# Performance work log

Measured on AMD Instinct MI355X. Metric: run time of the kernel, lower is better.

## Reference

```python
import jax, jax.numpy as jnp
import numpy as np

EPS = 1e-5

def fps(xyz, npoint):
    # iterative farthest point sampling, deterministic start at index 0
    B, N, _ = xyz.shape
    def step(carry, _):
        distance, farthest = carry
        centroid = jnp.take_along_axis(xyz, farthest[:, None, None], axis=1)  # [B,1,3]
        dist = jnp.sum((xyz - centroid) ** 2, -1)                              # [B,N]
        distance = jnp.minimum(distance, dist)
        new_far = jnp.argmax(distance, -1)
        return (distance, new_far), farthest
    init = (jnp.full((B, N), 1e10, xyz.dtype), jnp.zeros((B,), jnp.int32))
    _, idx = jax.lax.scan(step, init, None, length=npoint)
    return idx.T  # [B, npoint]

def gather_points(points, idx):
    # points [B,N,C], idx [B,S] or [B,S,K] -> gathered along N
    B = points.shape[0]
    if idx.ndim == 2:
        return jnp.take_along_axis(points, idx[..., None], axis=1)
    S, K = idx.shape[1], idx.shape[2]
    flat = jnp.take_along_axis(points, idx.reshape(B, S * K)[..., None], axis=1)
    return flat.reshape(B, S, K, points.shape[-1])

def conv_bn_relu(x, W, b, gamma, beta):
    # x [B,C,K,S]; 1x1 conv = channel matmul; BN over (B,K,S) with batch stats
    y = jnp.einsum('bcks,oc->boks', x, W) + b[None, :, None, None]
    mean = jnp.mean(y, axis=(0, 2, 3), keepdims=True)
    var = jnp.mean((y - mean) ** 2, axis=(0, 2, 3), keepdims=True)
    y = (y - mean) * jax.lax.rsqrt(var + EPS)
    y = y * gamma[None, :, None, None] + beta[None, :, None, None]
    return jax.nn.relu(y)

NPOINT = 1024
NSAMPLE = 16

def setup_inputs() -> dict:
    key = jax.random.key(0)
    ks = jax.random.split(key, 6)
    B, N, D = 16, 4096, 128
    C_in, C1, C2 = D + 3, 256, 256
    xyz = jax.random.normal(ks[0], (B, N, 3), dtype=jnp.float32)
    points = jax.random.normal(ks[1], (B, N, D), dtype=jnp.float32)
    W1 = jax.random.normal(ks[2], (C1, C_in), dtype=jnp.float32) / np.sqrt(C_in)
    b1 = jnp.zeros((C1,), jnp.float32)
    g1 = jnp.ones((C1,), jnp.float32)
    bt1 = jnp.zeros((C1,), jnp.float32)
    W2 = jax.random.normal(ks[3], (C2, C1), dtype=jnp.float32) / np.sqrt(C1)
    b2 = jnp.zeros((C2,), jnp.float32)
    g2 = jnp.ones((C2,), jnp.float32)
    bt2 = jnp.zeros((C2,), jnp.float32)
    return {"xyz": xyz, "points": points, "W1": W1, "b1": b1, "g1": g1, "bt1": bt1,
            "W2": W2, "b2": b2, "g2": g2, "bt2": bt2}

def reference(xyz, points, W1, b1, g1, bt1, W2, b2, g2, bt2):
    B, N, _ = xyz.shape
    S, K = NPOINT, NSAMPLE
    fps_idx = fps(xyz, S)                       # [B,S]
    new_xyz = gather_points(xyz, fps_idx)       # [B,S,3]
    # kNN via squared distances
    d = jnp.sum((new_xyz[:, :, None] - xyz[:, None]) ** 2, -1)  # [B,S,N]
    _, idx = jax.lax.top_k(-d, K)                                # [B,S,K]
    grouped_xyz = gather_points(xyz, idx) - new_xyz[:, :, None]  # [B,S,K,3]
    grouped_pts = gather_points(points, idx)                     # [B,S,K,D]
    feat = jnp.concatenate([grouped_xyz, grouped_pts], -1)       # [B,S,K,3+D]
    x = jnp.transpose(feat, (0, 3, 2, 1))                        # [B,C,K,S]
    x = conv_bn_relu(x, W1, b1, g1, bt1)
    x = conv_bn_relu(x, W2, b2, g2, bt2)
    new_points = jnp.max(x, axis=2).transpose(0, 2, 1)           # [B,S,C2]
    return (new_xyz, new_points)
```

## Files before the change

kernel.cpp:

```cpp
#include <hip/hip_runtime.h>
#include <hip/hip_bf16.h>
#include <cstdint>
#include <cstddef>

#define BB   16
#define NN   4096
#define DD   128
#define SS   1024
#define CIN  131
#define C1   256
#define MM   (SS*16)

#define FP 168
#define AP 264

typedef __attribute__((ext_vector_type(8))) short bf16x8;
typedef __attribute__((ext_vector_type(4))) float f32x4;

__device__ __forceinline__ float bf2f(unsigned short u) {
  union { unsigned int i; float f; } x; x.i = ((unsigned int)u) << 16; return x.f;
}
__device__ __forceinline__ unsigned short f2bf(float f) {
  union { __hip_bfloat16 h; unsigned short u; } c; c.h = __float2bfloat16(f); return c.u;
}

__global__ __launch_bounds__(256) void convert_kernel(
    const float* __restrict__ W1, const float* __restrict__ W2,
    unsigned short* __restrict__ W1b, unsigned short* __restrict__ W2b)
{
  const int n = blockIdx.x, t = threadIdx.x;
  if (t < 160) {
    float v = 0.0f;
    if (t < 128)      v = W1[n*CIN + 3 + t];
    else if (t < 131) v = W1[n*CIN + (t - 128)];
    W1b[n*160 + t] = f2bf(v);
  }
  W2b[n*256 + t] = f2bf(W2[n*256 + t]);
}

__global__ __launch_bounds__(256) void fps_kernel(
    const float* __restrict__ xyz, float* __restrict__ out_xyz)
{
  __shared__ float xs[NN], ys[NN], zs[NN];
  __shared__ unsigned long long wres[2][4];
  const int b = blockIdx.x;
  const int tid = threadIdx.x;
  const int wave = tid >> 6, lane = tid & 63;
  const float* base = xyz + (size_t)b * NN * 3;
  for (int i = tid; i < NN; i += 256) {
    xs[i] = base[i*3+0]; ys[i] = base[i*3+1]; zs[i] = base[i*3+2];
  }
  __syncthreads();
  float px[16], py[16], pz[16], mind[16];
  #pragma unroll
  for (int j = 0; j < 16; ++j) {
    px[j] = xs[j*256 + tid];
    py[j] = ys[j*256 + tid];
    pz[j] = zs[j*256 + tid];
    mind[j] = 1e10f;
  }
  int far = 0;
  for (int it = 0; it < SS; ++it) {
    if (tid == 0) {
      out_xyz[(b*SS + it)*3 + 0] = xs[far];
      out_xyz[(b*SS + it)*3 + 1] = ys[far];
      out_xyz[(b*SS + it)*3 + 2] = zs[far];
    }
    const float cx = xs[far], cy = ys[far], cz = zs[far];
    float bv = -1.0f; int bj = 0;
    #pragma unroll
    for (int j = 0; j < 16; ++j) {
      float dx = __fsub_rn(px[j], cx);
      float dy = __fsub_rn(py[j], cy);
      float dz = __fsub_rn(pz[j], cz);
      float d  = __fadd_rn(__fadd_rn(__fmul_rn(dx,dx), __fmul_rn(dy,dy)), __fmul_rn(dz,dz));
      float md = fminf(mind[j], d);
      mind[j] = md;
      if (md > bv) { bv = md; bj = j; }
    }
    unsigned long long best = ((unsigned long long)__float_as_uint(bv) << 32)
                            | (unsigned int)(~(unsigned int)(bj*256 + tid));
    #define FPS_STEP(CTRL) { \
      unsigned int lo = (unsigned int)best, hi = (unsigned int)(best >> 32); \
      unsigned int lo2 = (unsigned int)__builtin_amdgcn_update_dpp((int)lo, (int)lo, CTRL, 0xf, 0xf, false); \
      unsigned int hi2 = (unsigned int)__builtin_amdgcn_update_dpp((int)hi, (int)hi, CTRL, 0xf, 0xf, false); \
      unsigned long long o = (((unsigned long long)hi2) << 32) | lo2; \
      if (o > best) best = o; }
    FPS_STEP(0x111) FPS_STEP(0x112) FPS_STEP(0x114) FPS_STEP(0x118)
    FPS_STEP(0x142) FPS_STEP(0x143)
    #undef FPS_STEP
    const int par = it & 1;
    if (lane == 63) wres[par][wave] = best;
    __syncthreads();
    unsigned long long g = wres[par][0];
    #pragma unroll
    for (int w = 1; w < 4; ++w) {
      unsigned long long o = wres[par][w];
      if (o > g) g = o;
    }
    far = (int)(~(unsigned int)g);
  }
}

__global__ __launch_bounds__(256) void knn_kernel(
    const float* __restrict__ xyz, const float* __restrict__ new_xyz, int* __restrict__ knn_idx)
{
  __shared__ __align__(16) float tile[12288];
  const int b = blockIdx.y;
  const int tid = threadIdx.x;
  const int q = tid >> 2, c = tid & 3;
  const int s = blockIdx.x * 64 + q;
  {
    const float4* src = (const float4*)(xyz + (size_t)b*NN*3);
    float4* dst = (float4*)tile;
    #pragma unroll
    for (int k = 0; k < 12; ++k) dst[tid + k*256] = src[tid + k*256];
  }
  const float cx = new_xyz[((b<<10)+s)*3+0];
  const float cy = new_xyz[((b<<10)+s)*3+1];
  const float cz = new_xyz[((b<<10)+s)*3+2];
  float td[16]; int ti[16];
  #pragma unroll
  for (int j = 0; j < 16; ++j) { td[j] = 3.4e38f; ti[j] = 0; }
  __syncthreads();
  const float* base = tile + c*3072;
  for (int i0 = 0; i0 < 1024; i0 += 8) {
    const float4 v0 = *(const float4*)&base[i0*3 +  0];
    const float4 v1 = *(const float4*)&base[i0*3 +  4];
    const float4 v2 = *(const float4*)&base[i0*3 +  8];
    const float4 v3 = *(const float4*)&base[i0*3 + 12];
    const float4 v4 = *(const float4*)&base[i0*3 + 16];
    const float4 v5 = *(const float4*)&base[i0*3 + 20];
    float d[8];
    #define KDIST(slot, X, Y, Z) { \
      float dx = __fsub_rn(X, cx); \
      float dy = __fsub_rn(Y, cy); \
      float dz = __fsub_rn(Z, cz); \
      d[slot] = __fadd_rn(__fadd_rn(__fmul_rn(dx,dx), __fmul_rn(dy,dy)), __fmul_rn(dz,dz)); }
    KDIST(0, v0.x, v0.y, v0.z)
    KDIST(1, v0.w, v1.x, v1.y)
    KDIST(2, v1.z, v1.w, v2.x)
    KDIST(3, v2.y, v2.z, v2.w)
    KDIST(4, v3.x, v3.y, v3.z)
    KDIST(5, v3.w, v4.x, v4.y)
    KDIST(6, v4.z, v4.w, v5.x)
    KDIST(7, v5.y, v5.z, v5.w)
    #undef KDIST
    #pragma unroll
    for (int j = 0; j < 8; ++j) {
      if (d[j] < td[15]) {
        td[15] = d[j]; ti[15] = c*1024 + i0 + j;
        #pragma unroll
        for (int p = 15; p > 0; --p) {
          if (td[p] < td[p-1]) {
            float tf = td[p]; td[p] = td[p-1]; td[p-1] = tf;
            int   tt = ti[p]; ti[p] = ti[p-1]; ti[p-1] = tt;
          }
        }
      }
    }
  }
  __syncthreads();
  float* dbuf = tile;
  int*   ibuf = (int*)(tile + 4352);
  #pragma unroll
  for (int j = 0; j < 16; ++j) { dbuf[tid*17 + j] = td[j]; ibuf[tid*17 + j] = ti[j]; }
  __syncthreads();
  if (c == 0) {
    int h0 = 0, h1 = 0, h2 = 0, h3 = 0;
    const int s0 = (q*4+0)*17, s1 = (q*4+1)*17, s2 = (q*4+2)*17, s3 = (q*4+3)*17;
    int* o = knn_idx + ((size_t)((b<<10)+s))*16;
    #pragma unroll
    for (int out = 0; out < 16; ++out) {
      float d0 = dbuf[s0+h0], d1 = dbuf[s1+h1], d2 = dbuf[s2+h2], d3 = dbuf[s3+h3];
      float bd = d0; int bc = 0;
      if (d1 < bd) { bd = d1; bc = 1; }
      if (d2 < bd) { bd = d2; bc = 2; }
      if (d3 < bd) { bd = d3; bc = 3; }
      int idx;
      if      (bc == 0) { idx = ibuf[s0+h0]; ++h0; }
      else if (bc == 1) { idx = ibuf[s1+h1]; ++h1; }
      else if (bc == 2) { idx = ibuf[s2+h2]; ++h2; }
      else              { idx = ibuf[s3+h3]; ++h3; }
      o[out] = idx;
    }
  }
}

__device__ __forceinline__ void stage_features(
    unsigned short* Fs, const float* xyz, const float* points,
    const int* knn_idx, const float* new_xyz, int b, int by, int tid)
{
  const int rg = tid >> 2, cg = tid & 3;
  const int m = by*64 + rg;
  const int s = m >> 4, kk = m & 15;
  const int p = knn_idx[((b<<10)+s)*16 + kk];
  const float4* pb = (const float4*)(points + ((size_t)b*NN + p) * DD);
  unsigned short* row = Fs + rg*FP;
  #pragma unroll
  for (int i = 0; i < 8; ++i) {
    float4 v = pb[cg*8 + i];
    ushort4 u;
    u.x = f2bf(v.x); u.y = f2bf(v.y); u.z = f2bf(v.z); u.w = f2bf(v.w);
    *(ushort4*)&row[cg*32 + i*4] = u;
  }
  if (cg == 0) {
    float c3[3];
    c3[0] = xyz[((size_t)b*NN + p)*3+0] - new_xyz[((b<<10)+s)*3+0];
    c3[1] = xyz[((size_t)b*NN + p)*3+1] - new_xyz[((b<<10)+s)*3+1];
    c3[2] = xyz[((size_t)b*NN + p)*3+2] - new_xyz[((b<<10)+s)*3+2];
    #pragma unroll
    for (int k = 128; k < 160; k += 4) {
      ushort4 u;
      u.x = f2bf(k+0 < 131 ? c3[k-128+0] : 0.0f);
      u.y = f2bf(k+1 < 131 ? c3[k-128+1] : 0.0f);
      u.z = f2bf(k+2 < 131 ? c3[k-128+2] : 0.0f);
      u.w = f2bf(k+3 < 131 ? c3[k-128+3] : 0.0f);
      *(ushort4*)&row[k] = u;
    }
  }
}

__global__ __launch_bounds__(256, 2) void gemm1_stats_kernel(
    const float* __restrict__ xyz, const float* __restrict__ points,
    const unsigned short* __restrict__ W1b, const float* __restrict__ bias1,
    const int* __restrict__ knn_idx, const float* __restrict__ new_xyz,
    float* __restrict__ Psum, float* __restrict__ Psq)
{
  __shared__ unsigned short Fs[64*FP];
  __shared__ float RedS[1024];
  __shared__ float RedQ[1024];
  const int by = blockIdx.x, b = blockIdx.y;
  const int tid = threadIdx.x;
  const int wave = tid >> 6, lane = tid & 63;
  const int m15 = lane & 15, quad = lane >> 4;
  const int n0w = wave * 64;

  stage_features(Fs, xyz, points, knn_idx, new_xyz, b, by, tid);
  __syncthreads();

  f32x4 acc[4][4];
  #pragma unroll
  for (int t = 0; t < 4; ++t)
    #pragma unroll
    for (int u = 0; u < 4; ++u) acc[t][u] = (f32x4){0.f,0.f,0.f,0.f};

  #pragma unroll
  for (int kc = 0; kc < 5; ++kc) {
    const int k0 = kc * 32;
    bf16x8 af[4], bfr[4];
    #pragma unroll
    for (int u = 0; u < 4; ++u)
      bfr[u] = *(const bf16x8*)&W1b[(size_t)(n0w + u*16 + m15)*160 + k0 + quad*8];
    #pragma unroll
    for (int t = 0; t < 4; ++t)
      af[t] = *(const bf16x8*)&Fs[(t*16 + m15)*FP + k0 + quad*8];
    #pragma unroll
    for (int t = 0; t < 4; ++t)
      #pragma unroll
      for (int u = 0; u < 4; ++u)
        acc[t][u] = __builtin_amdgcn_mfma_f32_16x16x32_bf16(af[t], bfr[u], acc[t][u], 0, 0, 0);
  }

  #pragma unroll
  for (int u = 0; u < 4; ++u) {
    const int n = n0w + u*16 + m15;
    const float bias = bias1[n];
    float ps = 0.f, pq = 0.f;
    #pragma unroll
    for (int t = 0; t < 4; ++t)
      #pragma unroll
      for (int r = 0; r < 4; ++r) {
        float y = acc[t][u][r] + bias;
        ps += y; pq += y*y;
      }
    RedS[n*4 + quad] = ps;
    RedQ[n*4 + quad] = pq;
  }
  __syncthreads();
  {
    const int n = tid;
    float4 s4 = *(const float4*)&RedS[n*4];
    float4 q4 = *(const float4*)&RedQ[n*4];
    const int row = b*256 + by;
    Psum[(size_t)n*4096 + row] = (s4.x + s4.y) + (s4.z + s4.w);
    Psq [(size_t)n*4096 + row] = (q4.x + q4.y) + (q4.z + q4.w);
  }
}

__global__ __launch_bounds__(256) void stats_kernel(
    const float* __restrict__ Psum, const float* __restrict__ Psq,
    const float* __restrict__ gamma, const float* __restrict__ beta,
    float* __restrict__ scale, float* __restrict__ shift)
{
  __shared__ float sv[4], qv[4];
  const int c = blockIdx.x, tid = threadIdx.x;
  float s = 0.f, q = 0.f;
  for (int r = tid; r < 4096; r += 256) { s += Psum[(size_t)c*4096+r]; q += Psq[(size_t)c*4096+r]; }
  #pragma unroll
  for (int off = 32; off > 0; off >>= 1) { s += __shfl_down(s, off); q += __shfl_down(q, off); }
  if ((tid & 63) == 0) { sv[tid>>6] = s; qv[tid>>6] = q; }
  __syncthreads();
  if (tid == 0) {
    s = sv[0]+sv[1]+sv[2]+sv[3]; q = qv[0]+qv[1]+qv[2]+qv[3];
    const float count = 262144.0f;
    float mean = s / count;
    float var  = fmaxf(q / count - mean*mean, 0.0f);
    float inv  = 1.0f / sqrtf(var + 1e-5f);
    float sc   = gamma[c] * inv;
    scale[c] = sc;
    shift[c] = beta[c] - mean * sc;
  }
}

__global__ __launch_bounds__(256, 2) void fused2_kernel(
    const float* __restrict__ xyz, const float* __restrict__ points,
    const unsigned short* __restrict__ W1b, const float* __restrict__ bias1,
    const int* __restrict__ knn_idx, const float* __restrict__ new_xyz,
    const float* __restrict__ sc1v, const float* __restrict__ sh1v,
    const unsigned short* __restrict__ W2b, const float* __restrict__ bias2,
    float* __restrict__ maxv, float* __restrict__ minv,
    float* __restrict__ Psum, float* __restrict__ Psq)
{
  __shared__ char smem[58368];
  unsigned short* As_  = (unsigned short*)smem;
  unsigned short* Fs   = (unsigned short*)smem;
  float* RedS  = (float*)(smem + 33792);
  float* RedQ  = (float*)(smem + 37888);
  float* MMBuf = (float*)(smem + 41984);

  const int by = blockIdx.x, b = blockIdx.y;
  const int tid = threadIdx.x;
  const int wave = tid >> 6, lane = tid & 63;
  const int m15 = lane & 15, quad = lane >> 4;
  const int n0w = wave * 64;

  stage_features(Fs, xyz, points, knn_idx, new_xyz, b, by, tid);
  __syncthreads();

  f32x4 acc[4][4];
  #pragma unroll
  for (int t = 0; t < 4; ++t)
    #pragma unroll
    for (int u = 0; u < 4; ++u) acc[t][u] = (f32x4){0.f,0.f,0.f,0.f};

  #pragma unroll
  for (int kc = 0; kc < 5; ++kc) {
    const int k0 = kc * 32;
    bf16x8 af[4], bfr[4];
    #pragma unroll
    for (int u = 0; u < 4; ++u)
      bfr[u] = *(const bf16x8*)&W1b[(size_t)(n0w + u*16 + m15)*160 + k0 + quad*8];
    #pragma unroll
    for (int t = 0; t < 4; ++t)
      af[t] = *(const bf16x8*)&Fs[(t*16 + m15)*FP + k0 + quad*8];
    #pragma unroll
    for (int t = 0; t < 4; ++t)
      #pragma unroll
      for (int u = 0; u < 4; ++u)
        acc[t][u] = __builtin_amdgcn_mfma_f32_16x16x32_bf16(af[t], bfr[u], acc[t][u], 0, 0, 0);
  }

  __syncthreads();

  #pragma unroll
  for (int u = 0; u < 4; ++u) {
    const int n = n0w + u*16 + m15;
    const float bias = bias1[n], sc = sc1v[n], sh = sh1v[n];
    #pragma unroll
    for (int t = 0; t < 4; ++t)
      #pragma unroll
      for (int r = 0; r < 4; ++r) {
        float a = fmaxf((acc[t][u][r] + bias)*sc + sh, 0.0f);
        As_[(t*16 + quad*4 + r)*AP + n] = f2bf(a);
      }
  }

  #pragma unroll
  for (int t = 0; t < 4; ++t)
    #pragma unroll
    for (int u = 0; u < 4; ++u) acc[t][u] = (f32x4){0.f,0.f,0.f,0.f};

  __syncthreads();

  #pragma unroll
  for (int kc = 0; kc < 8; ++kc) {
    const int k0 = kc * 32;
    bf16x8 af[4], bfr[4];
    #pragma unroll
    for (int u = 0; u < 4; ++u)
      bfr[u] = *(const bf16x8*)&W2b[(size_t)(n0w + u*16 + m15)*256 + k0 + quad*8];
    #pragma unroll
    for (int t = 0; t < 4; ++t)
      af[t] = *(const bf16x8*)&As_[(t*16 + m15)*AP + k0 + quad*8];
    #pragma unroll
    for (int t = 0; t < 4; ++t)
      #pragma unroll
      for (int u = 0; u < 4; ++u)
        acc[t][u] = __builtin_amdgcn_mfma_f32_16x16x32_bf16(af[t], bfr[u], acc[t][u], 0, 0, 0);
  }

  float mxv[4][4], mnv[4][4];
  #pragma unroll
  for (int u = 0; u < 4; ++u) {
    const int n = n0w + u*16 + m15;
    const float bias = bias2[n];
    float ps = 0.f, pq = 0.f;
    #pragma unroll
    for (int t = 0; t < 4; ++t) {
      float y0 = acc[t][u][0] + bias, y1 = acc[t][u][1] + bias;
      float y2 = acc[t][u][2] + bias, y3 = acc[t][u][3] + bias;
      ps += ((y0 + y1) + (y2 + y3));
      pq += ((y0*y0 + y1*y1) + (y2*y2 + y3*y3));
      mxv[t][u] = fmaxf(fmaxf(y0, y1), fmaxf(y2, y3));
      mnv[t][u] = fminf(fminf(y0, y1), fminf(y2, y3));
    }
    RedS[n*4 + quad] = ps;
    RedQ[n*4 + quad] = pq;
    #pragma unroll
    for (int t = 0; t < 4; ++t) MMBuf[(t*256 + n)*4 + quad] = mxv[t][u];
  }
  __syncthreads();
  {
    const int n = tid;
    float4 s4 = *(const float4*)&RedS[n*4];
    float4 q4 = *(const float4*)&RedQ[n*4];
    const int row = b*256 + by;
    Psum[(size_t)n*4096 + row] = (s4.x + s4.y) + (s4.z + s4.w);
    Psq [(size_t)n*4096 + row] = (q4.x + q4.y) + (q4.z + q4.w);
    #pragma unroll
    for (int j = 0; j < 4; ++j) {
      float4 m4 = *(const float4*)&MMBuf[(j*256 + n)*4];
      float v = fmaxf(fmaxf(m4.x, m4.y), fmaxf(m4.z, m4.w));
      maxv[((size_t)((b<<10) + by*4 + j))*C1 + n] = v;
    }
  }
  __syncthreads();
  #pragma unroll
  for (int u = 0; u < 4; ++u) {
    const int n = n0w + u*16 + m15;
    #pragma unroll
    for (int t = 0; t < 4; ++t) MMBuf[(t*256 + n)*4 + quad] = mnv[t][u];
  }
  __syncthreads();
  {
    const int n = tid;
    #pragma unroll
    for (int j = 0; j < 4; ++j) {
      float4 m4 = *(const float4*)&MMBuf[(j*256 + n)*4];
      float v = fminf(fminf(m4.x, m4.y), fminf(m4.z, m4.w));
      minv[((size_t)((b<<10) + by*4 + j))*C1 + n] = v;
    }
  }
}

__global__ __launch_bounds__(256) void final_kernel(
    const float* __restrict__ maxv, const float* __restrict__ minv,
    const float* __restrict__ scale2, const float* __restrict__ shift2,
    float* __restrict__ out)
{
  const int bs = blockIdx.x;
  const int n  = threadIdx.x;
  const float sc = scale2[n], sh = shift2[n];
  const size_t idx = (size_t)bs * C1 + n;
  const float sel = (sc >= 0.0f) ? maxv[idx] : minv[idx];
  out[(size_t)BB*SS*3 + idx] = fmaxf(sc*sel + sh, 0.0f);
}

extern "C" void kernel_launch(void* const* d_in, const int* in_sizes, int n_in,
                              void* d_out, int out_size, void* d_ws, size_t ws_size,
                              hipStream_t stream) {
  const float* xyz    = (const float*)d_in[0];
  const float* points = (const float*)d_in[1];
  const float* W1     = (const float*)d_in[2];
  const float* b1     = (const float*)d_in[3];
  const float* g1     = (const float*)d_in[4];
  const float* bt1    = (const float*)d_in[5];
  const float* W2     = (const float*)d_in[6];
  const float* b2     = (const float*)d_in[7];
  const float* g2     = (const float*)d_in[8];
  const float* bt2    = (const float*)d_in[9];
  float* out = (float*)d_out;
  char* ws = (char*)d_ws;

  int*   knn_idx = (int*)(ws + 0);
  float* Ps      = (float*)(ws + 1048576ULL);
  float* Pq      = (float*)(ws + 5242880ULL);
  float* sc1     = (float*)(ws + 9437184ULL);
  float* sh1     = (float*)(ws + 9438208ULL);
  float* sc2     = (float*)(ws + 9439232ULL);
  float* sh2     = (float*)(ws + 9440256ULL);
  float* maxv    = (float*)(ws + 9441280ULL);
  float* minv    = (float*)(ws + 26218496ULL);
  unsigned short* W1b = (unsigned short*)(ws + 42995712ULL);
  unsigned short* W2b = (unsigned short*)(ws + 43077632ULL);

  float* new_xyz = out;

  convert_kernel<<<256, 256, 0, stream>>>(W1, W2, W1b, W2b);
  fps_kernel<<<BB, 256, 0, stream>>>(xyz, new_xyz);
  knn_kernel<<<dim3(16, BB), 256, 0, stream>>>(xyz, new_xyz, knn_idx);
  gemm1_stats_kernel<<<dim3(256, BB), 256, 0, stream>>>(xyz, points, W1b, b1, knn_idx, new_xyz, Ps, Pq);
  stats_kernel<<<256, 256, 0, stream>>>(Ps, Pq, g1, bt1, sc1, sh1);
  fused2_kernel<<<dim3(256, BB), 256, 0, stream>>>(xyz, points, W1b, b1, knn_idx, new_xyz,
                                                   sc1, sh1, W2b, b2, maxv, minv, Ps, Pq);
  stats_kernel<<<256, 256, 0, stream>>>(Ps, Pq, g2, bt2, sc2, sh2);
  final_kernel<<<BB*SS, 256, 0, stream>>>(maxv, minv, sc2, sh2, out);
}
```

Baseline: 1.091 ms.

## Process two batches per FPS block and drop shared-memory point staging

The farthest-point-sampling kernel now handles two batch elements per block, interleaving their distance updates and DPP reductions to raise instruction-level parallelism. It halves the grid size. The shared-memory copy of xyz is removed: points are loaded straight into registers, and each new centroid is fetched from global memory after the block-wide argmax. This doubles the per-thread register footprint and puts a global-load latency on the serial critical path of every iteration.

```diff
diff --git a/kernel.cpp b/kernel.cpp
--- a/kernel.cpp
+++ b/kernel.cpp
@@ -41,64 +41,78 @@
 __global__ __launch_bounds__(256) void fps_kernel(
     const float* __restrict__ xyz, float* __restrict__ out_xyz)
 {
-  __shared__ float xs[NN], ys[NN], zs[NN];
-  __shared__ unsigned long long wres[2][4];
-  const int b = blockIdx.x;
+  __shared__ unsigned long long wres[2][2][4];
+  const int blk = blockIdx.x;
+  const int bA = blk*2, bB = blk*2 + 1;
   const int tid = threadIdx.x;
   const int wave = tid >> 6, lane = tid & 63;
-  const float* base = xyz + (size_t)b * NN * 3;
-  for (int i = tid; i < NN; i += 256) {
-    xs[i] = base[i*3+0]; ys[i] = base[i*3+1]; zs[i] = base[i*3+2];
-  }
-  __syncthreads();
-  float px[16], py[16], pz[16], mind[16];
+  const float* baseA = xyz + (size_t)bA*NN*3;
+  const float* baseB = xyz + (size_t)bB*NN*3;
+  float pxA[16], pyA[16], pzA[16], mindA[16];
+  float pxB[16], pyB[16], pzB[16], mindB[16];
   #pragma unroll
   for (int j = 0; j < 16; ++j) {
-    px[j] = xs[j*256 + tid];
-    py[j] = ys[j*256 + tid];
-    pz[j] = zs[j*256 + tid];
-    mind[j] = 1e10f;
-  }
-  int far = 0;
+    const int p = (j*256 + tid)*3;
+    pxA[j] = baseA[p+0]; pyA[j] = baseA[p+1]; pzA[j] = baseA[p+2]; mindA[j] = 1e10f;
+    pxB[j] = baseB[p+0]; pyB[j] = baseB[p+1]; pzB[j] = baseB[p+2]; mindB[j] = 1e10f;
+  }
+  float cxA = baseA[0], cyA = baseA[1], czA = baseA[2];
+  float cxB = baseB[0], cyB = baseB[1], czB = baseB[2];
+  float* outA = out_xyz + (size_t)bA*SS*3;
+  float* outB = out_xyz + (size_t)bB*SS*3;
   for (int it = 0; it < SS; ++it) {
     if (tid == 0) {
-      out_xyz[(b*SS + it)*3 + 0] = xs[far];
-      out_xyz[(b*SS + it)*3 + 1] = ys[far];
-      out_xyz[(b*SS + it)*3 + 2] = zs[far];
-    }
-    const float cx = xs[far], cy = ys[far], cz = zs[far];
-    float bv = -1.0f; int bj = 0;
+      outA[it*3+0] = cxA; outA[it*3+1] = cyA; outA[it*3+2] = czA;
+      outB[it*3+0] = cxB; outB[it*3+1] = cyB; outB[it*3+2] = czB;
+    }
+    float bvA = -1.0f, bvB = -1.0f; int bjA = 0, bjB = 0;
     #pragma unroll
     for (int j = 0; j < 16; ++j) {
-      float dx = __fsub_rn(px[j], cx);
-      float dy = __fsub_rn(py[j], cy);
-      float dz = __fsub_rn(pz[j], cz);
-      float d  = __fadd_rn(__fadd_rn(__fmul_rn(dx,dx), __fmul_rn(dy,dy)), __fmul_rn(dz,dz));
-      float md = fminf(mind[j], d);
-      mind[j] = md;
-      if (md > bv) { bv = md; bj = j; }
-    }
-    unsigned long long best = ((unsigned long long)__float_as_uint(bv) << 32)
-                            | (unsigned int)(~(unsigned int)(bj*256 + tid));
-    #define FPS_STEP(CTRL) { \
-      unsigned int lo = (unsigned int)best, hi = (unsigned int)(best >> 32); \
-      unsigned int lo2 = (unsigned int)__builtin_amdgcn_update_dpp((int)lo, (int)lo, CTRL, 0xf, 0xf, false); \
-      unsigned int hi2 = (unsigned int)__builtin_amdgcn_update_dpp((int)hi, (int)hi, CTRL, 0xf, 0xf, false); \
-      unsigned long long o = (((unsigned long long)hi2) << 32) | lo2; \
-      if (o > best) best = o; }
-    FPS_STEP(0x111) FPS_STEP(0x112) FPS_STEP(0x114) FPS_STEP(0x118)
-    FPS_STEP(0x142) FPS_STEP(0x143)
-    #undef FPS_STEP
+      {
+        float dx = __fsub_rn(pxA[j], cxA);
+        float dy = __fsub_rn(pyA[j], cyA);
+        float dz = __fsub_rn(pzA[j], czA);
+        float d  = __fadd_rn(__fadd_rn(__fmul_rn(dx,dx), __fmul_rn(dy,dy)), __fmul_rn(dz,dz));
+        float md = fminf(mindA[j], d); mindA[j] = md;
+        if (md > bvA) { bvA = md; bjA = j; }
+      }
+      {
+        float dx = __fsub_rn(pxB[j], cxB);
+        float dy = __fsub_rn(pyB[j], cyB);
+        float dz = __fsub_rn(pzB[j], czB);
+        float d  = __fadd_rn(__fadd_rn(__fmul_rn(dx,dx), __fmul_rn(dy,dy)), __fmul_rn(dz,dz));
+        float md = fminf(mindB[j], d); mindB[j] = md;
+        if (md > bvB) { bvB = md; bjB = j; }
+      }
+    }
+    unsigned long long kA = (((unsigned long long)__float_as_uint(bvA)) << 32)
+                          | (unsigned int)(~(unsigned int)(bjA*256 + tid));
+    unsigned long long kB = (((unsigned long long)__float_as_uint(bvB)) << 32)
+                          | (unsigned int)(~(unsigned int)(bjB*256 + tid));
+    #define STEP2(CTRL) { \
+      { unsigned int lo = (unsigned int)kA, hi = (unsigned int)(kA >> 32); \
+        unsigned int lo2 = (unsigned int)__builtin_amdgcn_update_dpp((int)lo, (int)lo, CTRL, 0xf, 0xf, false); \
+        unsigned int hi2 = (unsigned int)__builtin_amdgcn_update_dpp((int)hi, (int)hi, CTRL, 0xf, 0xf, false); \
+        unsigned long long o = (((unsigned long long)hi2) << 32) | lo2; if (o > kA) kA = o; } \
+      { unsigned int lo = (unsigned int)kB, hi = (unsigned int)(kB >> 32); \
+        unsigned int lo2 = (unsigned int)__builtin_amdgcn_update_dpp((int)lo, (int)lo, CTRL, 0xf, 0xf, false); \
+        unsigned int hi2 = (unsigned int)__builtin_amdgcn_update_dpp((int)hi, (int)hi, CTRL, 0xf, 0xf, false); \
+        unsigned long long o = (((unsigned long long)hi2) << 32) | lo2; if (o > kB) kB = o; } }
+    STEP2(0x111) STEP2(0x112) STEP2(0x114) STEP2(0x118) STEP2(0x142) STEP2(0x143)
+    #undef STEP2
     const int par = it & 1;
-    if (lane == 63) wres[par][wave] = best;
+    if (lane == 63) { wres[par][0][wave] = kA; wres[par][1][wave] = kB; }
     __syncthreads();
-    unsigned long long g = wres[par][0];
+    unsigned long long gA = wres[par][0][0], gB = wres[par][1][0];
     #pragma unroll
     for (int w = 1; w < 4; ++w) {
-      unsigned long long o = wres[par][w];
-      if (o > g) g = o;
-    }
-    far = (int)(~(unsigned int)g);
+      unsigned long long oA = wres[par][0][w]; if (oA > gA) gA = oA;
+      unsigned long long oB = wres[par][1][w]; if (oB > gB) gB = oB;
+    }
+    const int farA = (int)(~(unsigned int)gA);
+    const int farB = (int)(~(unsigned int)gB);
+    cxA = baseA[farA*3+0]; cyA = baseA[farA*3+1]; czA = baseA[farA*3+2];
+    cxB = baseB[farB*3+0]; cyB = baseB[farB*3+1]; czB = baseB[farB*3+2];
   }
 }
 
@@ -498,7 +512,7 @@
   float* new_xyz = out;
 
   convert_kernel<<<256, 256, 0, stream>>>(W1, W2, W1b, W2b);
-  fps_kernel<<<BB, 256, 0, stream>>>(xyz, new_xyz);
+  fps_kernel<<<BB/2, 256, 0, stream>>>(xyz, new_xyz);
   knn_kernel<<<dim3(16, BB), 256, 0, stream>>>(xyz, new_xyz, knn_idx);
   gemm1_stats_kernel<<<dim3(256, BB), 256, 0, stream>>>(xyz, points, W1b, b1, knn_idx, new_xyz, Ps, Pq);
   stats_kernel<<<256, 256, 0, stream>>>(Ps, Pq, g1, bt1, sc1, sh1);
```

Result: slower. 1.667 ms (+52.8%).
